# Optimization experiments

Hardware: AMD Instinct MI355X
Metric: run time of the kernel (lower is better)

The kernel has to match this reference:

```python
import jax, jax.numpy as jnp
import numpy as np

D = 2048        # d_model
H = 16          # n_heads
HKV = 4         # n_kv_heads
DH = 128        # d_head = D // H
FF = int(D * 8 / 3)  # 5461, SwiGLU hidden
EPS = 1e-6
ROPE_BASE = 10000.0
B, L = 2, 2048


def rmsnorm(x, w):
    rms = jnp.sqrt(jnp.mean(x * x, axis=-1, keepdims=True) + EPS)
    return x / rms * w


def rope_cos_sin(seq_len):
    inv_freq = 1.0 / (ROPE_BASE ** (jnp.arange(0, DH, 2, dtype=jnp.float32) / DH))
    t = jnp.arange(seq_len, dtype=jnp.float32)
    freqs = t[:, None] * inv_freq[None, :]              # (L, DH/2)
    emb = jnp.concatenate([freqs, freqs], axis=-1)      # (L, DH)
    return jnp.cos(emb), jnp.sin(emb)


def rotate_half(x):
    x1, x2 = jnp.split(x, 2, axis=-1)
    return jnp.concatenate([-x2, x1], axis=-1)


def setup_inputs() -> dict:
    key = jax.random.key(0)
    ks = jax.random.split(key, 10)
    s = 0.02
    return {
        "x": jax.random.normal(ks[0], (B, L, D), dtype=jnp.float32),
        "w_norm1": jnp.ones((D,), dtype=jnp.float32),
        "wq": jax.random.normal(ks[1], (D, H * DH), dtype=jnp.float32) * s,
        "wk": jax.random.normal(ks[2], (D, HKV * DH), dtype=jnp.float32) * s,
        "wv": jax.random.normal(ks[3], (D, HKV * DH), dtype=jnp.float32) * s,
        "wo": jax.random.normal(ks[4], (H * DH, D), dtype=jnp.float32) * s,
        "w_norm2": jnp.ones((D,), dtype=jnp.float32),
        "w_gate": jax.random.normal(ks[5], (D, FF), dtype=jnp.float32) * s,
        "w_up": jax.random.normal(ks[6], (D, FF), dtype=jnp.float32) * s,
        "w_down": jax.random.normal(ks[7], (FF, D), dtype=jnp.float32) * s,
    }


def reference(x, w_norm1, wq, wk, wv, wo, w_norm2, w_gate, w_up, w_down):
    b, l, d = x.shape
    n_rep = H // HKV
    residual = x
    h = rmsnorm(x, w_norm1)
    q = (h @ wq).reshape(b, l, H, DH).transpose(0, 2, 1, 3)    # (B,H,L,DH)
    k = (h @ wk).reshape(b, l, HKV, DH).transpose(0, 2, 1, 3)  # (B,HKV,L,DH)
    v = (h @ wv).reshape(b, l, HKV, DH).transpose(0, 2, 1, 3)
    cos, sin = rope_cos_sin(l)                                 # (L,DH), broadcasts
    q = q * cos + rotate_half(q) * sin
    k = k * cos + rotate_half(k) * sin
    # GQA: repeat KV heads to match Q heads
    k = jnp.repeat(k, n_rep, axis=1)
    v = jnp.repeat(v, n_rep, axis=1)
    scale = 1.0 / np.sqrt(DH)
    attn = jnp.einsum('bhld,bhmd->bhlm', q, k) * scale         # (B,H,L,L)
    causal = jnp.triu(jnp.ones((l, l), dtype=bool), 1)
    attn = jnp.where(causal, -1e9, attn)
    attn = jax.nn.softmax(attn, axis=-1)
    out = jnp.einsum('bhlm,bhmd->bhld', attn, v)
    out = out.transpose(0, 2, 1, 3).reshape(b, l, d)
    x = residual + out @ wo
    residual = x
    h = rmsnorm(x, w_norm2)
    ffn = (jax.nn.silu(h @ w_gate) * (h @ w_up)) @ w_down
    return residual + ffn
```

## Files before the change

### kernel.cpp

```cpp
#include <hip/hip_runtime.h>
#include <stdint.h>

#define BATCH 2
#define SEQ   2048
#define DM    2048
#define NH    16
#define NKV   4
#define DHD   128
#define FFR   5461
#define FFP   5504
#define NTOK  (BATCH*SEQ)
#define QKVW  3072

typedef float f32x4 __attribute__((ext_vector_type(4)));
typedef short bf8v __attribute__((ext_vector_type(8)));
typedef unsigned short us8 __attribute__((ext_vector_type(8)));

__device__ __forceinline__ unsigned short f2bf(float f) {
  unsigned u = __float_as_uint(f);
  u += 0x7fff + ((u >> 16) & 1);
  return (unsigned short)(u >> 16);
}
__device__ __forceinline__ float bf2f(unsigned short b) {
  return __uint_as_float(((unsigned)b) << 16);
}

__device__ __forceinline__ void gload16(const void* g, void* l) {
  __builtin_amdgcn_global_load_lds(
      (const __attribute__((address_space(1))) unsigned int*)(uintptr_t)g,
      (__attribute__((address_space(3))) unsigned int*)(uintptr_t)l,
      16, 0, 0);
}

__global__ __launch_bounds__(256) void k_transpose(const float* __restrict__ S,
    unsigned short* __restrict__ T, int K, int N, int Kpad)
{
  __shared__ float tile[32][33];
  const int n0 = blockIdx.x << 5, k0 = blockIdx.y << 5;
  const int c = threadIdx.x & 31, r0 = threadIdx.x >> 5;
#pragma unroll
  for (int i = 0; i < 4; ++i) {
    int r = r0 + (i << 3);
    float v = 0.f;
    if ((k0 + r) < K && (n0 + c) < N) v = S[(long)(k0 + r) * N + n0 + c];
    tile[r][c] = v;
  }
  __syncthreads();
#pragma unroll
  for (int i = 0; i < 4; ++i) {
    int rr = r0 + (i << 3);
    T[(long)(n0 + rr) * Kpad + k0 + c] = f2bf(tile[c][rr]);
  }
}

__global__ __launch_bounds__(256) void k_transpose_v(const unsigned short* __restrict__ KV,
    unsigned short* __restrict__ VT)
{
  __shared__ unsigned short tile[32][36];
  const int kv0 = blockIdx.x << 5, d0 = blockIdx.y << 5;
  const int bz = blockIdx.z;
  const int b = bz >> 2, hkv = bz & 3;
  const int flat = threadIdx.x * 4;
  const int r = flat >> 5, c = flat & 31;
  ushort4 v = *(const ushort4*)(KV + ((long)(b*SEQ + kv0 + r))*QKVW + 2560 + hkv*128 + d0 + c);
  tile[r][c] = v.x; tile[r][c+1] = v.y; tile[r][c+2] = v.z; tile[r][c+3] = v.w;
  __syncthreads();
  ushort4 o;
  o.x = tile[c][r]; o.y = tile[c+1][r]; o.z = tile[c+2][r]; o.w = tile[c+3][r];
  *(ushort4*)(VT + ((long)(bz*128 + d0 + r))*SEQ + kv0 + c) = o;
}

__global__ __launch_bounds__(256) void k_rmsnorm(const float* __restrict__ X,
    const float* __restrict__ W, unsigned short* __restrict__ H)
{
  __shared__ float red[4];
  const long row = blockIdx.x;
  const float* xr = X + row * DM;
  const int tid = threadIdx.x;
  float4 a0 = ((const float4*)xr)[2*tid];
  float4 a1 = ((const float4*)xr)[2*tid+1];
  float ss = a0.x*a0.x + a0.y*a0.y + a0.z*a0.z + a0.w*a0.w
           + a1.x*a1.x + a1.y*a1.y + a1.z*a1.z + a1.w*a1.w;
#pragma unroll
  for (int m = 32; m >= 1; m >>= 1) ss += __shfl_xor(ss, m, 64);
  if ((tid & 63) == 0) red[tid >> 6] = ss;
  __syncthreads();
  float sc = rsqrtf((red[0]+red[1]+red[2]+red[3]) * (1.0f/DM) + 1e-6f);
  float4 w0 = ((const float4*)W)[2*tid];
  float4 w1 = ((const float4*)W)[2*tid+1];
  us8 o;
  o[0]=f2bf(a0.x*sc*w0.x); o[1]=f2bf(a0.y*sc*w0.y); o[2]=f2bf(a0.z*sc*w0.z); o[3]=f2bf(a0.w*sc*w0.w);
  o[4]=f2bf(a1.x*sc*w1.x); o[5]=f2bf(a1.y*sc*w1.y); o[6]=f2bf(a1.z*sc*w1.z); o[7]=f2bf(a1.w*sc*w1.w);
  *(us8*)(H + row*DM + tid*8) = o;
}

__global__ void k_rope_table(float* __restrict__ C, float* __restrict__ S)
{
  int i = blockIdx.x * 256 + threadIdx.x;
  int pos = i >> 6, d = i & 63;
  double inv = exp(-(double)d * (9.210340371976184 / 64.0));
  double ang = (double)pos * inv;
  C[i] = (float)cos(ang);
  S[i] = (float)sin(ang);
}

__global__ __launch_bounds__(256) void k_rope_apply(unsigned short* __restrict__ Q,
    const float* __restrict__ C, const float* __restrict__ S, int nh, int stride, int head0)
{
  long i = (long)blockIdx.x * 256 + threadIdx.x;
  int d = (int)(i & 63);
  long t = i >> 6;
  int hh = (int)(t % nh);
  long bl = t / nh;
  int pos = (int)(bl & (SEQ-1));
  long base = bl * stride + head0 + hh*DHD;
  float c = C[pos*64 + d], s = S[pos*64 + d];
  float x1 = bf2f(Q[base + d]);
  float x2 = bf2f(Q[base + 64 + d]);
  Q[base + d]      = f2bf(x1*c - x2*s);
  Q[base + 64 + d] = f2bf(x2*c + x1*s);
}

template<int EPI>
__global__ __launch_bounds__(256) void k_gemm(const unsigned short* __restrict__ A,
    const unsigned short* __restrict__ BT, void* Cout, const float* __restrict__ Res,
    const unsigned short* __restrict__ Gin, int K, int ldc)
{
  __shared__ __align__(16) unsigned short As[2][128*64];
  __shared__ __align__(16) unsigned short Bs[2][128*64];
  const int tid = threadIdx.x;
  const int l = tid & 63, w = tid >> 6;
  const int wr = w >> 1, wc = w & 1;
  const int nM = gridDim.x, nN = gridDim.y;
  const int nwg = nM * nN;
  const int bid = blockIdx.y * gridDim.x + blockIdx.x;
  const int q8 = nwg >> 3, r8 = nwg & 7, xcd = bid & 7, off8 = bid >> 3;
  const int wg = (xcd < r8 ? xcd*(q8+1) : r8*(q8+1) + (xcd - r8)*q8) + off8;
  const int colTiles = nM * 4;
  const int fullCols = nN >> 2, rem = nN & 3;
  int sc, inCol, wN;
  if (wg < fullCols * colTiles) { sc = wg / colTiles; inCol = wg % colTiles; wN = 4; }
  else { sc = fullCols; inCol = wg - fullCols * colTiles; wN = rem; }
  const int perSuper = 2 * wN;
  const int sm = inCol / perSuper, t8 = inCol % perSuper;
  const long m0 = (long)(sm*2 + t8 / wN) * 128;
  const long n0 = (long)(sc*4 + t8 % wN) * 128;
  const char* Ab = (const char*)(A + m0 * (long)K);
  const char* Bb = (const char*)(BT + n0 * (long)K);
  f32x4 acc[4][4] = {};
  const long ldab = (long)K * 2;
  const int nk = K >> 6;
  const int srow = w*32 + (l >> 3);
  const int scol = ((l & 7) ^ (srow & 7)) * 16;
  auto STAGE = [&](int buf, int kt) {
    const long kb = (long)kt * 128;
#pragma unroll
    for (int i = 0; i < 4; ++i) {
      gload16(Ab + (long)(srow + i*8)*ldab + kb + scol, &As[buf][(w*32 + i*8)*64]);
      gload16(Bb + (long)(srow + i*8)*ldab + kb + scol, &Bs[buf][(w*32 + i*8)*64]);
    }
  };
  STAGE(0, 0);
  __syncthreads();
  int cur = 0;
  for (int kt = 0; kt < nk; ++kt) {
    if (kt + 1 < nk) STAGE(cur ^ 1, kt + 1);
#pragma unroll
    for (int kk = 0; kk < 2; ++kk) {
      bf8v af[4], bfv[4];
#pragma unroll
      for (int m = 0; m < 4; ++m) {
        int r = wr*64 + m*16 + (l & 15);
        int offb = (kk*64 + (l >> 4)*16) ^ ((r & 7) << 4);
        af[m] = *(const bf8v*)((const char*)&As[cur][0] + r*128 + offb);
      }
#pragma unroll
      for (int n = 0; n < 4; ++n) {
        int cI = wc*64 + n*16 + (l & 15);
        int offb = (kk*64 + (l >> 4)*16) ^ ((cI & 7) << 4);
        bfv[n] = *(const bf8v*)((const char*)&Bs[cur][0] + cI*128 + offb);
      }
#pragma unroll
      for (int m = 0; m < 4; ++m)
#pragma unroll
        for (int n = 0; n < 4; ++n)
          acc[m][n] = __builtin_amdgcn_mfma_f32_16x16x32_bf16(af[m], bfv[n], acc[m][n], 0, 0, 0);
    }
    __syncthreads();
    cur ^= 1;
  }
#pragma unroll
  for (int m = 0; m < 4; ++m)
#pragma unroll
    for (int n = 0; n < 4; ++n)
#pragma unroll
      for (int r = 0; r < 4; ++r) {
        long row = m0 + wr*64 + m*16 + (l >> 4)*4 + r;
        long col = n0 + wc*64 + n*16 + (l & 15);
        long idx = row * (long)ldc + col;
        if (EPI == 0) ((unsigned short*)Cout)[idx] = f2bf(acc[m][n][r]);
        else if (EPI == 1) ((float*)Cout)[idx] = Res[idx] + acc[m][n][r];
        else {
          float g = bf2f(Gin[idx]);
          float sv = g / (1.f + __expf(-g));
          ((unsigned short*)Cout)[idx] = f2bf(sv * acc[m][n][r]);
        }
      }
}

__global__ __launch_bounds__(512) void k_attn(const unsigned short* __restrict__ QKV,
    const unsigned short* __restrict__ VbT, unsigned short* __restrict__ O)
{
  __shared__ __align__(16) unsigned short Ks[2][64*128];
  __shared__ __align__(16) unsigned short Vs[2][128*64];
  __shared__ __align__(16) unsigned short Pl[8][16][64];
  const int tid = threadIdx.x, l = tid & 63, w = tid >> 6;
  const int b = blockIdx.z, h = blockIdx.y;
  const int hkv = h >> 2;
  const float scale = 0.08838834764831845f;
  const unsigned short* Kbase = QKV + (long)b*SEQ*QKVW + 2048 + hkv*128;
  const unsigned short* Vtb = VbT + ((long)(b*NKV + hkv))*128*SEQ;

  for (int half = 0; half < 2; ++half) {
    const int qt = half ? (15 - (int)blockIdx.x) : (int)blockIdx.x;
    const int q0 = qt << 7;
    bf8v qa[4];
    {
      const unsigned short* qp = QKV + ((long)(b*SEQ + q0 + w*16 + (l & 15)))*QKVW + h*DHD + (l >> 4)*8;
#pragma unroll
      for (int kk = 0; kk < 4; ++kk) qa[kk] = *(const bf8v*)(qp + kk*32);
    }
    float m_[4], s_[4];
    f32x4 o_[8] = {};
#pragma unroll
    for (int r = 0; r < 4; ++r) { m_[r] = -1e30f; s_[r] = 0.f; }
    const int T = 2*qt + 2;
    const int qmaxw = q0 + w*16 + 15;

    auto STAGE = [&](int buf, int t) {
      const int kv0 = t << 6;
#pragma unroll
      for (int i = 0; i < 2; ++i) {
        int r = w*8 + i*4 + (l >> 4);
        int blk = (l & 15) ^ (r & 7);
        gload16(Kbase + ((long)(kv0 + r))*QKVW + blk*8, &Ks[buf][(w*8 + i*4)*128]);
      }
#pragma unroll
      for (int i = 0; i < 2; ++i) {
        int r = w*16 + i*8 + (l >> 3);
        int blk = (l & 7) ^ (r & 7);
        gload16(Vtb + (long)r*SEQ + kv0 + blk*8, &Vs[buf][(w*16 + i*8)*64]);
      }
    };
    STAGE(0, 0);
    __syncthreads();
    int cur = 0;
    for (int t = 0; t < T; ++t) {
      const int kv0 = t << 6;
      if (t + 1 < T) STAGE(cur ^ 1, t + 1);
      if (kv0 <= qmaxw) {
        f32x4 sc4[4] = {};
#pragma unroll
        for (int n = 0; n < 4; ++n) {
          int row = n*16 + (l & 15);
          const char* kr = (const char*)&Ks[cur][0] + row*256;
#pragma unroll
          for (int kk = 0; kk < 4; ++kk) {
            int off = (kk*64 + (l >> 4)*16) ^ ((row & 7) << 4);
            bf8v kf = *(const bf8v*)(kr + off);
            sc4[n] = __builtin_amdgcn_mfma_f32_16x16x32_bf16(qa[kk], kf, sc4[n], 0, 0, 0);
          }
        }
        float p[4][4];
        float rmax[4] = {-3e30f, -3e30f, -3e30f, -3e30f};
#pragma unroll
        for (int n = 0; n < 4; ++n) {
          int kv = kv0 + n*16 + (l & 15);
#pragma unroll
          for (int r = 0; r < 4; ++r) {
            int qr = q0 + w*16 + (l >> 4)*4 + r;
            float v = sc4[n][r] * scale;
            if (kv > qr) v = -1e30f;
            p[n][r] = v;
            rmax[r] = fmaxf(rmax[r], v);
          }
        }
#pragma unroll
        for (int r = 0; r < 4; ++r) {
          rmax[r] = fmaxf(rmax[r], __shfl_xor(rmax[r], 1, 64));
          rmax[r] = fmaxf(rmax[r], __shfl_xor(rmax[r], 2, 64));
          rmax[r] = fmaxf(rmax[r], __shfl_xor(rmax[r], 4, 64));
          rmax[r] = fmaxf(rmax[r], __shfl_xor(rmax[r], 8, 64));
        }
        float alpha[4], ps[4];
#pragma unroll
        for (int r = 0; r < 4; ++r) {
          float mn = fmaxf(m_[r], rmax[r]);
          alpha[r] = __expf(m_[r] - mn);
          m_[r] = mn;
          ps[r] = 0.f;
        }
#pragma unroll
        for (int n = 0; n < 4; ++n)
#pragma unroll
          for (int r = 0; r < 4; ++r) {
            float e = __expf(p[n][r] - m_[r]);
            p[n][r] = e;
            ps[r] += e;
          }
#pragma unroll
        for (int r = 0; r < 4; ++r) {
          ps[r] += __shfl_xor(ps[r], 1, 64);
          ps[r] += __shfl_xor(ps[r], 2, 64);
          ps[r] += __shfl_xor(ps[r], 4, 64);
          ps[r] += __shfl_xor(ps[r], 8, 64);
          s_[r] = s_[r]*alpha[r] + ps[r];
        }
#pragma unroll
        for (int g = 0; g < 8; ++g) {
          o_[g][0] *= alpha[0]; o_[g][1] *= alpha[1];
          o_[g][2] *= alpha[2]; o_[g][3] *= alpha[3];
        }
#pragma unroll
        for (int n = 0; n < 4; ++n)
#pragma unroll
          for (int r = 0; r < 4; ++r)
            Pl[w][(l >> 4)*4 + r][n*16 + (l & 15)] = f2bf(p[n][r]);
#pragma unroll
        for (int kk2 = 0; kk2 < 2; ++kk2) {
          bf8v pa = *(const bf8v*)&Pl[w][l & 15][kk2*32 + (l >> 4)*8];
#pragma unroll
          for (int g = 0; g < 8; ++g) {
            int d = g*16 + (l & 15);
            int off = (kk2*64 + (l >> 4)*16) ^ ((d & 7) << 4);
            bf8v vf = *(const bf8v*)((const char*)&Vs[cur][0] + d*128 + off);
            o_[g] = __builtin_amdgcn_mfma_f32_16x16x32_bf16(pa, vf, o_[g], 0, 0, 0);
          }
        }
      }
      __syncthreads();
      cur ^= 1;
    }
#pragma unroll
    for (int g = 0; g < 8; ++g)
#pragma unroll
      for (int r = 0; r < 4; ++r) {
        long row = (long)b*SEQ + q0 + w*16 + (l >> 4)*4 + r;
        O[row*DM + h*DHD + g*16 + (l & 15)] = f2bf(o_[g][r] / s_[r]);
      }
  }
}

extern "C" void kernel_launch(void* const* d_in, const int* in_sizes, int n_in,
                              void* d_out, int out_size, void* d_ws, size_t ws_size,
                              hipStream_t stream)
{
  const float* x   = (const float*)d_in[0];
  const float* wn1 = (const float*)d_in[1];
  const float* wq  = (const float*)d_in[2];
  const float* wk  = (const float*)d_in[3];
  const float* wv  = (const float*)d_in[4];
  const float* wo  = (const float*)d_in[5];
  const float* wn2 = (const float*)d_in[6];
  const float* wg  = (const float*)d_in[7];
  const float* wu  = (const float*)d_in[8];
  const float* wd  = (const float*)d_in[9];
  float* out = (float*)d_out;

  char* p = (char*)d_ws;
  auto alloc = [&](size_t bytes) { char* r = p; p += (bytes + 255) & ~(size_t)255; return r; };
  unsigned short* wqkvT = (unsigned short*)alloc((size_t)QKVW*2048*2);
  unsigned short* woT  = (unsigned short*)alloc((size_t)2048*2048*2);
  unsigned short* wgT  = (unsigned short*)alloc((size_t)FFP*2048*2);
  unsigned short* wuT  = (unsigned short*)alloc((size_t)FFP*2048*2);
  unsigned short* wdT  = (unsigned short*)alloc((size_t)2048*FFP*2);
  unsigned short* hb   = (unsigned short*)alloc((size_t)NTOK*2048*2);
  unsigned short* pr   = (unsigned short*)alloc((size_t)NTOK*FFP*2);
  char* scratch = p;
  unsigned short* qkv  = (unsigned short*)alloc((size_t)NTOK*QKVW*2);
  unsigned short* vbT  = (unsigned short*)alloc((size_t)BATCH*NKV*128*SEQ*2);
  unsigned short* ao   = (unsigned short*)alloc((size_t)NTOK*2048*2);
  float* ctab = (float*)alloc((size_t)SEQ*64*4);
  float* stab = (float*)alloc((size_t)SEQ*64*4);
  unsigned short* gb   = (unsigned short*)scratch;

  dim3 blk(256);
  k_transpose<<<dim3(2048/32, 2048/32), blk, 0, stream>>>(wq, wqkvT, 2048, 2048, 2048);
  k_transpose<<<dim3(512/32,  2048/32), blk, 0, stream>>>(wk, wqkvT + (size_t)2048*2048, 2048, 512, 2048);
  k_transpose<<<dim3(512/32,  2048/32), blk, 0, stream>>>(wv, wqkvT + (size_t)2560*2048, 2048, 512, 2048);
  k_transpose<<<dim3(2048/32, 2048/32), blk, 0, stream>>>(wo, woT, 2048, 2048, 2048);
  k_transpose<<<dim3(FFP/32,  2048/32), blk, 0, stream>>>(wg, wgT, 2048, FFR, 2048);
  k_transpose<<<dim3(FFP/32,  2048/32), blk, 0, stream>>>(wu, wuT, 2048, FFR, 2048);
  k_transpose<<<dim3(2048/32, FFP/32),  blk, 0, stream>>>(wd, wdT, FFR, 2048, FFP);

  k_rope_table<<<dim3(SEQ*64/256), blk, 0, stream>>>(ctab, stab);
  k_rmsnorm<<<dim3(NTOK), blk, 0, stream>>>(x, wn1, hb);

  k_gemm<0><<<dim3(32, QKVW/128), blk, 0, stream>>>(hb, wqkvT, qkv, nullptr, nullptr, 2048, QKVW);

  k_rope_apply<<<dim3(NTOK*NH*64/256),  blk, 0, stream>>>(qkv, ctab, stab, NH, QKVW, 0);
  k_rope_apply<<<dim3(NTOK*NKV*64/256), blk, 0, stream>>>(qkv, ctab, stab, NKV, QKVW, 2048);

  k_transpose_v<<<dim3(SEQ/32, 128/32, BATCH*NKV), blk, 0, stream>>>(qkv, vbT);

  k_attn<<<dim3(8, NH, BATCH), dim3(512), 0, stream>>>(qkv, vbT, ao);

  k_gemm<1><<<dim3(32, 16), blk, 0, stream>>>(ao, woT, (void*)out, x, nullptr, 2048, 2048);
  k_rmsnorm<<<dim3(NTOK), blk, 0, stream>>>(out, wn2, hb);
  k_gemm<0><<<dim3(32, FFP/128), blk, 0, stream>>>(hb, wgT, gb, nullptr, nullptr, 2048, FFP);
  k_gemm<2><<<dim3(32, FFP/128), blk, 0, stream>>>(hb, wuT, pr, nullptr, gb, 2048, FFP);
  k_gemm<1><<<dim3(32, 16), blk, 0, stream>>>(pr, wdT, (void*)out, out, nullptr, FFP, 2048);
}
```

Baseline: 692.0 us.

## Enlarge GEMM tiles to 256x256 with 8 waves and fine-grained interleaved pipeline

```diff
diff --git a/kernel.cpp b/kernel.cpp
--- a/kernel.cpp
+++ b/kernel.cpp
@@ -8,7 +8,7 @@
 #define NKV   4
 #define DHD   128
 #define FFR   5461
-#define FFP   5504
+#define FFP   5632
 #define NTOK  (BATCH*SEQ)
 #define QKVW  3072
 
@@ -122,15 +122,15 @@
 }
 
 template<int EPI>
-__global__ __launch_bounds__(256) void k_gemm(const unsigned short* __restrict__ A,
+__global__ __launch_bounds__(512) void k_gemm(const unsigned short* __restrict__ A,
     const unsigned short* __restrict__ BT, void* Cout, const float* __restrict__ Res,
     const unsigned short* __restrict__ Gin, int K, int ldc)
 {
-  __shared__ __align__(16) unsigned short As[2][128*64];
-  __shared__ __align__(16) unsigned short Bs[2][128*64];
-  const int tid = threadIdx.x;
-  const int l = tid & 63, w = tid >> 6;
-  const int wr = w >> 1, wc = w & 1;
+  __shared__ __align__(16) unsigned short As[2][2][256][32];
+  __shared__ __align__(16) unsigned short Bs[2][2][256][32];
+  const int tid = threadIdx.x, l = tid & 63, w = tid >> 6;
+  const int wr = w >> 2, wc = w & 3;
+  const int la = l & 15;
   const int nM = gridDim.x, nN = gridDim.y;
   const int nwg = nM * nN;
   const int bid = blockIdx.y * gridDim.x + blockIdx.x;
@@ -138,65 +138,99 @@
   const int wg = (xcd < r8 ? xcd*(q8+1) : r8*(q8+1) + (xcd - r8)*q8) + off8;
   const int colTiles = nM * 4;
   const int fullCols = nN >> 2, rem = nN & 3;
-  int sc, inCol, wN;
-  if (wg < fullCols * colTiles) { sc = wg / colTiles; inCol = wg % colTiles; wN = 4; }
-  else { sc = fullCols; inCol = wg - fullCols * colTiles; wN = rem; }
+  int sc_, inCol, wN;
+  if (wg < fullCols * colTiles) { sc_ = wg / colTiles; inCol = wg % colTiles; wN = 4; }
+  else { sc_ = fullCols; inCol = wg - fullCols * colTiles; wN = rem; }
   const int perSuper = 2 * wN;
   const int sm = inCol / perSuper, t8 = inCol % perSuper;
-  const long m0 = (long)(sm*2 + t8 / wN) * 128;
-  const long n0 = (long)(sc*4 + t8 % wN) * 128;
+  const long m0 = (long)(sm*2 + t8 / wN) * 256;
+  const long n0 = (long)(sc_*4 + t8 % wN) * 256;
   const char* Ab = (const char*)(A + m0 * (long)K);
   const char* Bb = (const char*)(BT + n0 * (long)K);
-  f32x4 acc[4][4] = {};
   const long ldab = (long)K * 2;
   const int nk = K >> 6;
-  const int srow = w*32 + (l >> 3);
-  const int scol = ((l & 7) ^ (srow & 7)) * 16;
-  auto STAGE = [&](int buf, int kt) {
-    const long kb = (long)kt * 128;
-#pragma unroll
-    for (int i = 0; i < 4; ++i) {
-      gload16(Ab + (long)(srow + i*8)*ldab + kb + scol, &As[buf][(w*32 + i*8)*64]);
-      gload16(Bb + (long)(srow + i*8)*ldab + kb + scol, &Bs[buf][(w*32 + i*8)*64]);
-    }
+  const int srow0 = w*16 + (l >> 2);
+  const int sbyte = ((l & 3) ^ ((l >> 2) & 3)) << 4;
+  const int jx = ((l >> 4) ^ (la & 3)) << 4;
+  const int aoff = (wr*128 + la)*64 + jx;
+  const int boff = (wc*64  + la)*64 + jx;
+
+  f32x4 acc[8][4] = {};
+  bf8v bv[4];
+
+  auto SA = [&](int buf, int kt, int kh) {
+    const long kb = (long)kt*128 + (long)kh*64;
+    char* ld = (char*)As + buf*32768 + kh*16384 + w*1024;
+    gload16(Ab + (long)srow0*ldab + kb + sbyte, ld);
+    gload16(Ab + (long)(srow0+128)*ldab + kb + sbyte, ld + 8192);
   };
-  STAGE(0, 0);
-  __syncthreads();
+  auto SB = [&](int buf, int kt, int kh) {
+    const long kb = (long)kt*128 + (long)kh*64;
+    char* ld = (char*)Bs + buf*32768 + kh*16384 + w*1024;
+    gload16(Bb + (long)srow0*ldab + kb + sbyte, ld);
+    gload16(Bb + (long)(srow0+128)*ldab + kb + sbyte, ld + 8192);
+  };
+
+#define GP(KH, MH, DOLDB, STG, VMW)                                           \
+  {                                                                           \
+    const char* pA = curA + (KH)*16384;                                       \
+    bf8v af[4];                                                               \
+    _Pragma("unroll")                                                         \
+    for (int mm = 0; mm < 4; ++mm)                                            \
+      af[mm] = *(const bf8v*)(pA + aoff + (MH)*4096 + mm*1024);               \
+    if (DOLDB) {                                                              \
+      const char* pB = curB + (KH)*16384;                                     \
+      _Pragma("unroll")                                                       \
+      for (int n = 0; n < 4; ++n)                                             \
+        bv[n] = *(const bf8v*)(pB + boff + n*1024);                           \
+    }                                                                         \
+    STG;                                                                      \
+    __builtin_amdgcn_sched_barrier(0);                                        \
+    __builtin_amdgcn_s_barrier();                                             \
+    asm volatile("s_waitcnt lgkmcnt(0)" ::: "memory");                        \
+    __builtin_amdgcn_sched_barrier(0);                                        \
+    __builtin_amdgcn_s_setprio(1);                                            \
+    _Pragma("unroll")                                                         \
+    for (int mm = 0; mm < 4; ++mm)                                            \
+      _Pragma("unroll")                                                       \
+      for (int n = 0; n < 4; ++n)                                             \
+        acc[(MH)*4+mm][n] = __builtin_amdgcn_mfma_f32_16x16x32_bf16(          \
+            af[mm], bv[n], acc[(MH)*4+mm][n], 0, 0, 0);                       \
+    __builtin_amdgcn_s_setprio(0);                                            \
+    VMW;                                                                      \
+    __builtin_amdgcn_s_barrier();                                             \
+  }
+
+  SA(0, 0, 0); SB(0, 0, 0); SA(0, 0, 1); SB(0, 0, 1);
+  asm volatile("s_waitcnt vmcnt(4)" ::: "memory");
+  __builtin_amdgcn_s_barrier();
+
   int cur = 0;
-  for (int kt = 0; kt < nk; ++kt) {
-    if (kt + 1 < nk) STAGE(cur ^ 1, kt + 1);
-#pragma unroll
-    for (int kk = 0; kk < 2; ++kk) {
-      bf8v af[4], bfv[4];
-#pragma unroll
-      for (int m = 0; m < 4; ++m) {
-        int r = wr*64 + m*16 + (l & 15);
-        int offb = (kk*64 + (l >> 4)*16) ^ ((r & 7) << 4);
-        af[m] = *(const bf8v*)((const char*)&As[cur][0] + r*128 + offb);
-      }
-#pragma unroll
-      for (int n = 0; n < 4; ++n) {
-        int cI = wc*64 + n*16 + (l & 15);
-        int offb = (kk*64 + (l >> 4)*16) ^ ((cI & 7) << 4);
-        bfv[n] = *(const bf8v*)((const char*)&Bs[cur][0] + cI*128 + offb);
-      }
-#pragma unroll
-      for (int m = 0; m < 4; ++m)
-#pragma unroll
-        for (int n = 0; n < 4; ++n)
-          acc[m][n] = __builtin_amdgcn_mfma_f32_16x16x32_bf16(af[m], bfv[n], acc[m][n], 0, 0, 0);
-    }
-    __syncthreads();
-    cur ^= 1;
+  for (int t = 0; t < nk; ++t) {
+    const bool more = (t + 1 < nk);
+    const int nxt = cur ^ 1;
+    const char* curA = (const char*)As + cur*32768;
+    const char* curB = (const char*)Bs + cur*32768;
+    GP(0, 0, 1, if (more) SA(nxt, t+1, 0), );
+    GP(0, 1, 0, if (more) SB(nxt, t+1, 0),
+       if (more) { asm volatile("s_waitcnt vmcnt(4)" ::: "memory"); }
+       else      { asm volatile("s_waitcnt vmcnt(0)" ::: "memory"); } );
+    GP(1, 0, 1, if (more) SA(nxt, t+1, 1), );
+    GP(1, 1, 0, if (more) SB(nxt, t+1, 1),
+       if (more) { asm volatile("s_waitcnt vmcnt(4)" ::: "memory"); }
+       else      { asm volatile("s_waitcnt vmcnt(0)" ::: "memory"); } );
+    cur = nxt;
   }
-#pragma unroll
-  for (int m = 0; m < 4; ++m)
+#undef GP
+
+#pragma unroll
+  for (int m = 0; m < 8; ++m)
 #pragma unroll
     for (int n = 0; n < 4; ++n)
 #pragma unroll
       for (int r = 0; r < 4; ++r) {
-        long row = m0 + wr*64 + m*16 + (l >> 4)*4 + r;
-        long col = n0 + wc*64 + n*16 + (l & 15);
+        long row = m0 + wr*128 + m*16 + (l >> 4)*4 + r;
+        long col = n0 + wc*64 + n*16 + la;
         long idx = row * (long)ldc + col;
         if (EPI == 0) ((unsigned short*)Cout)[idx] = f2bf(acc[m][n][r]);
         else if (EPI == 1) ((float*)Cout)[idx] = Res[idx] + acc[m][n][r];
@@ -396,7 +430,7 @@
   k_rope_table<<<dim3(SEQ*64/256), blk, 0, stream>>>(ctab, stab);
   k_rmsnorm<<<dim3(NTOK), blk, 0, stream>>>(x, wn1, hb);
 
-  k_gemm<0><<<dim3(32, QKVW/128), blk, 0, stream>>>(hb, wqkvT, qkv, nullptr, nullptr, 2048, QKVW);
+  k_gemm<0><<<dim3(16, QKVW/256), dim3(512), 0, stream>>>(hb, wqkvT, qkv, nullptr, nullptr, 2048, QKVW);
 
   k_rope_apply<<<dim3(NTOK*NH*64/256),  blk, 0, stream>>>(qkv, ctab, stab, NH, QKVW, 0);
   k_rope_apply<<<dim3(NTOK*NKV*64/256), blk, 0, stream>>>(qkv, ctab, stab, NKV, QKVW, 2048);
@@ -405,9 +439,9 @@
 
   k_attn<<<dim3(8, NH, BATCH), dim3(512), 0, stream>>>(qkv, vbT, ao);
 
-  k_gemm<1><<<dim3(32, 16), blk, 0, stream>>>(ao, woT, (void*)out, x, nullptr, 2048, 2048);
+  k_gemm<1><<<dim3(16, 8), dim3(512), 0, stream>>>(ao, woT, (void*)out, x, nullptr, 2048, 2048);
   k_rmsnorm<<<dim3(NTOK), blk, 0, stream>>>(out, wn2, hb);
-  k_gemm<0><<<dim3(32, FFP/128), blk, 0, stream>>>(hb, wgT, gb, nullptr, nullptr, 2048, FFP);
-  k_gemm<2><<<dim3(32, FFP/128), blk, 0, stream>>>(hb, wuT, pr, nullptr, gb, 2048, FFP);
-  k_gemm<1><<<dim3(32, 16), blk, 0, stream>>>(pr, wdT, (void*)out, out, nullptr, FFP, 2048);
-}
+  k_gemm<0><<<dim3(16, FFP/256), dim3(512), 0, stream>>>(hb, wgT, gb, nullptr, nullptr, 2048, FFP);
+  k_gemm<2><<<dim3(16, FFP/256), dim3(512), 0, stream>>>(hb, wuT, pr, nullptr, gb, 2048, FFP);
+  k_gemm<1><<<dim3(16, 8), dim3(512), 0, stream>>>(pr, wdT, (void*)out, out, nullptr, FFP, 2048);
+}
```

After: 876.4 us. +26.6%, slower.

## Add 256x256-tile 512-thread GEMM with 8 waves for QKV, O and FFN projections

Applied to the files above, without the earlier changes.

```diff
diff --git a/kernel.cpp b/kernel.cpp
--- a/kernel.cpp
+++ b/kernel.cpp
@@ -8,7 +8,7 @@
 #define NKV   4
 #define DHD   128
 #define FFR   5461
-#define FFP   5504
+#define FFP   5632
 #define NTOK  (BATCH*SEQ)
 #define QKVW  3072
 
@@ -122,7 +122,133 @@
 }
 
 template<int EPI>
-__global__ __launch_bounds__(256) void k_gemm(const unsigned short* __restrict__ A,
+__global__ __launch_bounds__(512) void k_gemm8(const unsigned short* __restrict__ A,
+    const unsigned short* __restrict__ BT, void* Cout, const float* __restrict__ Res,
+    const unsigned short* __restrict__ Gin, int K, int ldc)
+{
+  __shared__ __align__(16) unsigned short As[2][256][64];
+  __shared__ __align__(16) unsigned short Bs[2][256][64];
+  const int tid = threadIdx.x, l = tid & 63, w = tid >> 6;
+  const int wr = w >> 2, wc = w & 3;
+  const int la = l & 15, q = l >> 4;
+  const int nM = gridDim.x, nN = gridDim.y;
+  const int nwg = nM * nN;
+  const int bid = blockIdx.y * gridDim.x + blockIdx.x;
+  const int q8 = nwg >> 3, r8 = nwg & 7, xcd = bid & 7, off8 = bid >> 3;
+  const int wg = (xcd < r8 ? xcd*(q8+1) : r8*(q8+1) + (xcd - r8)*q8) + off8;
+  const int colTiles = nM * 4;
+  const int fullCols = nN >> 2, rem = nN & 3;
+  int sc_, inCol, wN;
+  if (wg < fullCols * colTiles) { sc_ = wg / colTiles; inCol = wg % colTiles; wN = 4; }
+  else { sc_ = fullCols; inCol = wg - fullCols * colTiles; wN = rem; }
+  const int perSuper = 2 * wN;
+  const int sm = inCol / perSuper, t8 = inCol % perSuper;
+  const long m0 = (long)(sm*2 + t8 / wN) * 256;
+  const long n0 = (long)(sc_*4 + t8 % wN) * 256;
+  const char* Ab = (const char*)(A + m0 * (long)K);
+  const char* Bb = (const char*)(BT + n0 * (long)K);
+  const long ldab = (long)K * 2;
+  const int nk = K >> 6;
+  const int srow8 = w*8 + (l >> 3);
+  const int sslot = ((l & 7) ^ ((l >> 3) & 7)) << 4;
+  const int arow = (wr*128 + la) * 128;
+  const int brow = (wc*64 + la) * 128;
+  const int sx0 = ((q ^ (la & 7)) << 4);
+  const int sx1 = (((4 + q) ^ (la & 7)) << 4);
+
+  f32x4 acc[8][4] = {};
+  bf8v bvv0[4], bvv1[4];
+
+  auto SA = [&](int buf, int kt, int mh) {
+    const long kb = (long)kt * 128;
+#pragma unroll
+    for (int i = 0; i < 2; ++i) {
+      int rblk = i*128 + mh*64;
+      gload16(Ab + (long)(rblk + srow8)*ldab + kb + sslot,
+              (char*)As + buf*32768 + rblk*128 + w*1024);
+    }
+  };
+  auto SB = [&](int buf, int kt, int h) {
+    const long kb = (long)kt * 128;
+#pragma unroll
+    for (int i = 0; i < 2; ++i) {
+      int rblk = h*128 + i*64;
+      gload16(Bb + (long)(rblk + srow8)*ldab + kb + sslot,
+              (char*)Bs + buf*32768 + rblk*128 + w*1024);
+    }
+  };
+
+#define GP(MH, BV, SX, LOADB, STG, VMW)                                       \
+  {                                                                           \
+    bf8v af[4];                                                               \
+    _Pragma("unroll")                                                         \
+    for (int mm = 0; mm < 4; ++mm)                                            \
+      af[mm] = *(const bf8v*)(curA + arow + (MH)*8192 + mm*2048 + (SX));      \
+    if (LOADB) {                                                              \
+      _Pragma("unroll")                                                       \
+      for (int n = 0; n < 4; ++n)                                             \
+        BV[n] = *(const bf8v*)(curB + brow + n*2048 + (SX));                  \
+    }                                                                         \
+    STG;                                                                      \
+    __builtin_amdgcn_sched_barrier(0);                                        \
+    __builtin_amdgcn_s_barrier();                                             \
+    asm volatile("s_waitcnt lgkmcnt(0)" ::: "memory");                        \
+    __builtin_amdgcn_sched_barrier(0);                                        \
+    __builtin_amdgcn_s_setprio(1);                                            \
+    _Pragma("unroll")                                                         \
+    for (int mm = 0; mm < 4; ++mm)                                            \
+      _Pragma("unroll")                                                       \
+      for (int n = 0; n < 4; ++n)                                             \
+        acc[(MH)*4+mm][n] = __builtin_amdgcn_mfma_f32_16x16x32_bf16(          \
+            af[mm], BV[n], acc[(MH)*4+mm][n], 0, 0, 0);                       \
+    __builtin_amdgcn_s_setprio(0);                                            \
+    VMW;                                                                      \
+    __builtin_amdgcn_s_barrier();                                             \
+  }
+
+  SB(0, 0, 0); SB(0, 0, 1); SA(0, 0, 0); SA(0, 0, 1);
+  asm volatile("s_waitcnt vmcnt(2)" ::: "memory");
+  __builtin_amdgcn_s_barrier();
+
+  int cur = 0;
+  for (int t = 0; t < nk; ++t) {
+    const bool more = (t + 1 < nk);
+    const int nxt = cur ^ 1;
+    const char* curA = (const char*)As + cur*32768;
+    const char* curB = (const char*)Bs + cur*32768;
+    GP(0, bvv0, sx0, 1, if (more) SB(nxt, t+1, 0), );
+    GP(0, bvv1, sx1, 1, if (more) SB(nxt, t+1, 1),
+       if (more) { asm volatile("s_waitcnt vmcnt(4)" ::: "memory"); }
+       else      { asm volatile("s_waitcnt vmcnt(0)" ::: "memory"); } );
+    GP(1, bvv0, sx0, 0, if (more) SA(nxt, t+1, 0), );
+    GP(1, bvv1, sx1, 0, if (more) SA(nxt, t+1, 1),
+       if (more) { asm volatile("s_waitcnt vmcnt(2)" ::: "memory"); }
+       else      { asm volatile("s_waitcnt vmcnt(0)" ::: "memory"); } );
+    cur = nxt;
+  }
+#undef GP
+
+#pragma unroll
+  for (int m = 0; m < 8; ++m)
+#pragma unroll
+    for (int n = 0; n < 4; ++n)
+#pragma unroll
+      for (int r = 0; r < 4; ++r) {
+        long row = m0 + wr*128 + m*16 + (l >> 4)*4 + r;
+        long col = n0 + wc*64 + n*16 + la;
+        long idx = row * (long)ldc + col;
+        if (EPI == 0) ((unsigned short*)Cout)[idx] = f2bf(acc[m][n][r]);
+        else if (EPI == 1) ((float*)Cout)[idx] = Res[idx] + acc[m][n][r];
+        else {
+          float g = bf2f(Gin[idx]);
+          float sv = g / (1.f + __expf(-g));
+          ((unsigned short*)Cout)[idx] = f2bf(sv * acc[m][n][r]);
+        }
+      }
+}
+
+template<int EPI>
+__global__ __launch_bounds__(256) void k_gemm2(const unsigned short* __restrict__ A,
     const unsigned short* __restrict__ BT, void* Cout, const float* __restrict__ Res,
     const unsigned short* __restrict__ Gin, int K, int ldc)
 {
@@ -396,7 +522,7 @@
   k_rope_table<<<dim3(SEQ*64/256), blk, 0, stream>>>(ctab, stab);
   k_rmsnorm<<<dim3(NTOK), blk, 0, stream>>>(x, wn1, hb);
 
-  k_gemm<0><<<dim3(32, QKVW/128), blk, 0, stream>>>(hb, wqkvT, qkv, nullptr, nullptr, 2048, QKVW);
+  k_gemm8<0><<<dim3(16, QKVW/256), dim3(512), 0, stream>>>(hb, wqkvT, qkv, nullptr, nullptr, 2048, QKVW);
 
   k_rope_apply<<<dim3(NTOK*NH*64/256),  blk, 0, stream>>>(qkv, ctab, stab, NH, QKVW, 0);
   k_rope_apply<<<dim3(NTOK*NKV*64/256), blk, 0, stream>>>(qkv, ctab, stab, NKV, QKVW, 2048);
@@ -405,9 +531,9 @@
 
   k_attn<<<dim3(8, NH, BATCH), dim3(512), 0, stream>>>(qkv, vbT, ao);
 
-  k_gemm<1><<<dim3(32, 16), blk, 0, stream>>>(ao, woT, (void*)out, x, nullptr, 2048, 2048);
+  k_gemm8<1><<<dim3(16, 8), dim3(512), 0, stream>>>(ao, woT, (void*)out, x, nullptr, 2048, 2048);
   k_rmsnorm<<<dim3(NTOK), blk, 0, stream>>>(out, wn2, hb);
-  k_gemm<0><<<dim3(32, FFP/128), blk, 0, stream>>>(hb, wgT, gb, nullptr, nullptr, 2048, FFP);
-  k_gemm<2><<<dim3(32, FFP/128), blk, 0, stream>>>(hb, wuT, pr, nullptr, gb, 2048, FFP);
-  k_gemm<1><<<dim3(32, 16), blk, 0, stream>>>(pr, wdT, (void*)out, out, nullptr, FFP, 2048);
-}
+  k_gemm8<0><<<dim3(16, FFP/256), dim3(512), 0, stream>>>(hb, wgT, gb, nullptr, nullptr, 2048, FFP);
+  k_gemm8<2><<<dim3(16, FFP/256), dim3(512), 0, stream>>>(hb, wuT, pr, nullptr, gb, 2048, FFP);
+  k_gemm2<1><<<dim3(32, 16), dim3(256), 0, stream>>>(pr, wdT, (void*)out, out, nullptr, FFP, 2048);
+}
```

After: 770.7 us. +11.4%, slower.

## Rework GEMM into 512-thread, 4-stage pipelined kernel with explicit vmcnt waits

Applied to the files above, without the earlier changes.

```diff
diff --git a/kernel.cpp b/kernel.cpp
--- a/kernel.cpp
+++ b/kernel.cpp
@@ -122,15 +122,15 @@
 }
 
 template<int EPI>
-__global__ __launch_bounds__(256) void k_gemm(const unsigned short* __restrict__ A,
+__global__ __launch_bounds__(512) void k_gemmc(const unsigned short* __restrict__ A,
     const unsigned short* __restrict__ BT, void* Cout, const float* __restrict__ Res,
     const unsigned short* __restrict__ Gin, int K, int ldc)
 {
-  __shared__ __align__(16) unsigned short As[2][128*64];
-  __shared__ __align__(16) unsigned short Bs[2][128*64];
-  const int tid = threadIdx.x;
-  const int l = tid & 63, w = tid >> 6;
-  const int wr = w >> 1, wc = w & 1;
+  __shared__ __align__(16) unsigned short As[4][128][64];
+  __shared__ __align__(16) unsigned short Bs[4][128][64];
+  const int tid = threadIdx.x, l = tid & 63, w = tid >> 6;
+  const int wr = w >> 2, wc = w & 3;
+  const int la = l & 15, q = l >> 4;
   const int nM = gridDim.x, nN = gridDim.y;
   const int nwg = nM * nN;
   const int bid = blockIdx.y * gridDim.x + blockIdx.x;
@@ -138,65 +138,72 @@
   const int wg = (xcd < r8 ? xcd*(q8+1) : r8*(q8+1) + (xcd - r8)*q8) + off8;
   const int colTiles = nM * 4;
   const int fullCols = nN >> 2, rem = nN & 3;
-  int sc, inCol, wN;
-  if (wg < fullCols * colTiles) { sc = wg / colTiles; inCol = wg % colTiles; wN = 4; }
-  else { sc = fullCols; inCol = wg - fullCols * colTiles; wN = rem; }
+  int sc_, inCol, wN;
+  if (wg < fullCols * colTiles) { sc_ = wg / colTiles; inCol = wg % colTiles; wN = 4; }
+  else { sc_ = fullCols; inCol = wg - fullCols * colTiles; wN = rem; }
   const int perSuper = 2 * wN;
   const int sm = inCol / perSuper, t8 = inCol % perSuper;
   const long m0 = (long)(sm*2 + t8 / wN) * 128;
-  const long n0 = (long)(sc*4 + t8 % wN) * 128;
+  const long n0 = (long)(sc_*4 + t8 % wN) * 128;
   const char* Ab = (const char*)(A + m0 * (long)K);
   const char* Bb = (const char*)(BT + n0 * (long)K);
-  f32x4 acc[4][4] = {};
   const long ldab = (long)K * 2;
   const int nk = K >> 6;
-  const int srow = w*32 + (l >> 3);
-  const int scol = ((l & 7) ^ (srow & 7)) * 16;
+  const int srow = w*8 + (l >> 3);
+  const int scol = ((l & 7) ^ ((l >> 3) & 7)) * 16;
+
   auto STAGE = [&](int buf, int kt) {
     const long kb = (long)kt * 128;
 #pragma unroll
-    for (int i = 0; i < 4; ++i) {
-      gload16(Ab + (long)(srow + i*8)*ldab + kb + scol, &As[buf][(w*32 + i*8)*64]);
-      gload16(Bb + (long)(srow + i*8)*ldab + kb + scol, &Bs[buf][(w*32 + i*8)*64]);
+    for (int i = 0; i < 2; ++i) {
+      gload16(Ab + (long)(i*64 + srow)*ldab + kb + scol, &As[buf][i*64 + w*8][0]);
+      gload16(Bb + (long)(i*64 + srow)*ldab + kb + scol, &Bs[buf][i*64 + w*8][0]);
     }
   };
-  STAGE(0, 0);
-  __syncthreads();
-  int cur = 0;
-  for (int kt = 0; kt < nk; ++kt) {
-    if (kt + 1 < nk) STAGE(cur ^ 1, kt + 1);
+
+  f32x4 acc[4][2] = {};
+
+  STAGE(0, 0); STAGE(1, 1); STAGE(2, 2);
+
+  for (int t = 0; t < nk; ++t) {
+    if (t + 2 < nk)      { asm volatile("s_waitcnt vmcnt(8)" ::: "memory"); }
+    else if (t + 1 < nk) { asm volatile("s_waitcnt vmcnt(4)" ::: "memory"); }
+    else                 { asm volatile("s_waitcnt vmcnt(0)" ::: "memory"); }
+    __builtin_amdgcn_s_barrier();
+    __builtin_amdgcn_sched_barrier(0);
+    if (t + 3 < nk) STAGE((t + 3) & 3, t + 3);
+    const int cb = t & 3;
 #pragma unroll
     for (int kk = 0; kk < 2; ++kk) {
-      bf8v af[4], bfv[4];
+      bf8v af[4], bfv[2];
 #pragma unroll
       for (int m = 0; m < 4; ++m) {
-        int r = wr*64 + m*16 + (l & 15);
-        int offb = (kk*64 + (l >> 4)*16) ^ ((r & 7) << 4);
-        af[m] = *(const bf8v*)((const char*)&As[cur][0] + r*128 + offb);
-      }
-#pragma unroll
-      for (int n = 0; n < 4; ++n) {
-        int cI = wc*64 + n*16 + (l & 15);
-        int offb = (kk*64 + (l >> 4)*16) ^ ((cI & 7) << 4);
-        bfv[n] = *(const bf8v*)((const char*)&Bs[cur][0] + cI*128 + offb);
+        int r = wr*64 + m*16 + la;
+        int offb = (kk*64 + q*16) ^ ((r & 7) << 4);
+        af[m] = *(const bf8v*)((const char*)&As[cb][0][0] + r*128 + offb);
+      }
+#pragma unroll
+      for (int n = 0; n < 2; ++n) {
+        int cI = wc*32 + n*16 + la;
+        int offb = (kk*64 + q*16) ^ ((cI & 7) << 4);
+        bfv[n] = *(const bf8v*)((const char*)&Bs[cb][0][0] + cI*128 + offb);
       }
 #pragma unroll
       for (int m = 0; m < 4; ++m)
 #pragma unroll
-        for (int n = 0; n < 4; ++n)
+        for (int n = 0; n < 2; ++n)
           acc[m][n] = __builtin_amdgcn_mfma_f32_16x16x32_bf16(af[m], bfv[n], acc[m][n], 0, 0, 0);
     }
-    __syncthreads();
-    cur ^= 1;
   }
+
 #pragma unroll
   for (int m = 0; m < 4; ++m)
 #pragma unroll
-    for (int n = 0; n < 4; ++n)
+    for (int n = 0; n < 2; ++n)
 #pragma unroll
       for (int r = 0; r < 4; ++r) {
-        long row = m0 + wr*64 + m*16 + (l >> 4)*4 + r;
-        long col = n0 + wc*64 + n*16 + (l & 15);
+        long row = m0 + wr*64 + m*16 + q*4 + r;
+        long col = n0 + wc*32 + n*16 + la;
         long idx = row * (long)ldc + col;
         if (EPI == 0) ((unsigned short*)Cout)[idx] = f2bf(acc[m][n][r]);
         else if (EPI == 1) ((float*)Cout)[idx] = Res[idx] + acc[m][n][r];
@@ -396,7 +403,7 @@
   k_rope_table<<<dim3(SEQ*64/256), blk, 0, stream>>>(ctab, stab);
   k_rmsnorm<<<dim3(NTOK), blk, 0, stream>>>(x, wn1, hb);
 
-  k_gemm<0><<<dim3(32, QKVW/128), blk, 0, stream>>>(hb, wqkvT, qkv, nullptr, nullptr, 2048, QKVW);
+  k_gemmc<0><<<dim3(32, QKVW/128), dim3(512), 0, stream>>>(hb, wqkvT, qkv, nullptr, nullptr, 2048, QKVW);
 
   k_rope_apply<<<dim3(NTOK*NH*64/256),  blk, 0, stream>>>(qkv, ctab, stab, NH, QKVW, 0);
   k_rope_apply<<<dim3(NTOK*NKV*64/256), blk, 0, stream>>>(qkv, ctab, stab, NKV, QKVW, 2048);
@@ -405,9 +412,9 @@
 
   k_attn<<<dim3(8, NH, BATCH), dim3(512), 0, stream>>>(qkv, vbT, ao);
 
-  k_gemm<1><<<dim3(32, 16), blk, 0, stream>>>(ao, woT, (void*)out, x, nullptr, 2048, 2048);
+  k_gemmc<1><<<dim3(32, 16), dim3(512), 0, stream>>>(ao, woT, (void*)out, x, nullptr, 2048, 2048);
   k_rmsnorm<<<dim3(NTOK), blk, 0, stream>>>(out, wn2, hb);
-  k_gemm<0><<<dim3(32, FFP/128), blk, 0, stream>>>(hb, wgT, gb, nullptr, nullptr, 2048, FFP);
-  k_gemm<2><<<dim3(32, FFP/128), blk, 0, stream>>>(hb, wuT, pr, nullptr, gb, 2048, FFP);
-  k_gemm<1><<<dim3(32, 16), blk, 0, stream>>>(pr, wdT, (void*)out, out, nullptr, FFP, 2048);
-}
+  k_gemmc<0><<<dim3(32, FFP/128), dim3(512), 0, stream>>>(hb, wgT, gb, nullptr, nullptr, 2048, FFP);
+  k_gemmc<2><<<dim3(32, FFP/128), dim3(512), 0, stream>>>(hb, wuT, pr, nullptr, gb, 2048, FFP);
+  k_gemmc<1><<<dim3(32, 16), dim3(512), 0, stream>>>(pr, wdT, (void*)out, out, nullptr, FFP, 2048);
+}
```

Result: slower. 726.2 us (+4.9%).
